# Kernel optimization log

Measured on AMD Instinct MI355X. Metric: run time of the kernel, lower is better.

## Reference

```python
import jax, jax.numpy as jnp
import numpy as np

B, T = 32, 1024
TEMP_IN, STAT_IN = 128, 64
TEMP_OUT, STAT_OUT = 128, 64
EPS = 1e-5
NEG_SLOPE = 0.01


def _bn_eval(x, gamma, beta, mean, var):
    # BatchNorm1d in eval mode (running stats)
    return (x - mean) * jax.lax.rsqrt(var + EPS) * gamma + beta


def _leaky_relu(x):
    return jnp.where(x >= 0, x, NEG_SLOPE * x)


def setup_inputs() -> dict:
    key = jax.random.key(0)
    k = jax.random.split(key, 6)
    # deterministic ragged lengths in [512, 1024]
    lengths_np = (512 + (np.arange(B) * 37) % 513).astype(np.int64)
    N = int(lengths_np.sum())  # 23450
    batch_idx = np.repeat(np.arange(B), lengths_np).astype(np.int32)
    pos_idx = np.concatenate([np.arange(l) for l in lengths_np]).astype(np.int32)
    valid = (np.arange(T)[None, :] < lengths_np[:, None])  # [B, T]
    mask_repeat = valid[:, :, None] & valid[:, None, :]    # [B, T, T]

    inp = {
        "x_temp": jax.random.normal(k[0], (N, TEMP_IN), jnp.float32),
        "x_stat": jax.random.normal(k[1], (B, STAT_IN), jnp.float32),
        "temp_attn": jax.random.normal(k[2], (B, T, T), jnp.float32) * 0.1,
        "mask_repeat": jnp.asarray(mask_repeat),
        "lengths": jnp.asarray(lengths_np),
        "batch_idx": jnp.asarray(batch_idx),
        "pos_idx": jnp.asarray(pos_idx),
        # non_linear_temp: Linear(TEMP_IN+STAT_IN -> TEMP_OUT) + BN
        "W1": jax.random.normal(k[3], (TEMP_OUT, TEMP_IN + STAT_IN), jnp.float32) / np.sqrt(TEMP_IN + STAT_IN),
        "b1": jnp.zeros((TEMP_OUT,), jnp.float32),
        "gamma1": jnp.ones((TEMP_OUT,), jnp.float32),
        "beta1": jnp.zeros((TEMP_OUT,), jnp.float32),
        "mean1": jnp.zeros((TEMP_OUT,), jnp.float32),
        "var1": jnp.ones((TEMP_OUT,), jnp.float32),
        # non_linear_stat: Linear(STAT_IN -> STAT_OUT) + BN
        "W2": jax.random.normal(k[4], (STAT_OUT, STAT_IN), jnp.float32) / np.sqrt(STAT_IN),
        "b2": jnp.zeros((STAT_OUT,), jnp.float32),
        "gamma2": jnp.ones((STAT_OUT,), jnp.float32),
        "beta2": jnp.zeros((STAT_OUT,), jnp.float32),
        "mean2": jnp.zeros((STAT_OUT,), jnp.float32),
        "var2": jnp.ones((STAT_OUT,), jnp.float32),
    }
    return inp


def reference(x_temp, x_stat, temp_attn, mask_repeat, lengths, batch_idx, pos_idx,
              W1, b1, gamma1, beta1, mean1, var1,
              W2, b2, gamma2, beta2, mean2, var2):
    # repeat_static_features: gather per-batch static feats to packed rows
    x_stat_rep = x_stat[batch_idx]                              # [N, STAT_IN]
    h = jnp.concatenate((x_temp, x_stat_rep), axis=-1) @ W1.T + b1
    h = _leaky_relu(_bn_eval(h, gamma1, beta1, mean1, var1))    # [N, TEMP_OUT]

    # pad_packed_sequences: scatter packed rows into [B, T, C] (zeros elsewhere)
    padded = jnp.zeros((B, T, TEMP_OUT), h.dtype).at[batch_idx, pos_idx].set(h)

    # self attention: softmax(x x^T / sqrt(d)) over padded rows (as original)
    d = jnp.asarray(TEMP_OUT, h.dtype)
    qk = jnp.einsum('btc,bsc->bts', padded, padded) / jnp.sqrt(d)
    self_attn = jax.nn.softmax(qk, axis=-1)

    attn = jnp.where(mask_repeat, self_attn + temp_attn, jnp.asarray(0.0, h.dtype))

    x_stat_out = _leaky_relu(_bn_eval(x_stat @ W2.T + b2, gamma2, beta2, mean2, var2))

    x_out_pad = jnp.einsum('bts,bsc->btc', attn, padded)        # [B, T, TEMP_OUT]
    # pack_padded_sequences: gather valid positions back to packed layout
    x_out = x_out_pad[batch_idx, pos_idx]                       # [N, TEMP_OUT]
    return (x_out, x_stat_out)
```

## Files before the change

kernel.cpp:

```cpp
#include <hip/hip_runtime.h>
#include <hip/hip_bf16.h>
#include <hip/hip_fp16.h>

typedef __hip_bfloat16 bf16;
typedef __attribute__((ext_vector_type(8))) short short8;
typedef __attribute__((ext_vector_type(4))) float f32x4;

#define EPS 1e-5f
#define NSLOPE 0.01f

__device__ __forceinline__ float b2f(bf16 v) { return __bfloat162float(v); }

__device__ __forceinline__ float ld1(const void* p, size_t idx, int isbf) {
  if (isbf) return b2f(((const bf16*)p)[idx]);
  return ((const float*)p)[idx];
}
__device__ __forceinline__ void st1(void* p, size_t idx, int isbf, float v) {
  if (isbf) ((bf16*)p)[idx] = __float2bfloat16(v);
  else      ((float*)p)[idx] = v;
}
__device__ __forceinline__ short f2bs(float x) {
  bf16 t = __float2bfloat16(x);
  short s; __builtin_memcpy(&s, &t, 2); return s;
}
__device__ __forceinline__ short8 pack8f(const float* p) {
  float4 a = *(const float4*)p, b = *(const float4*)(p + 4);
  short8 r;
  r[0] = f2bs(a.x); r[1] = f2bs(a.y); r[2] = f2bs(a.z); r[3] = f2bs(a.w);
  r[4] = f2bs(b.x); r[5] = f2bs(b.y); r[6] = f2bs(b.z); r[7] = f2bs(b.w);
  return r;
}

__global__ void meta_kernel(const void* __restrict__ xt,
                            const int* __restrict__ bidx, const int* __restrict__ pidx,
                            int N, int B, int* __restrict__ rs, int* __restrict__ ln,
                            int* __restrict__ flag,
                            const void* __restrict__ W1, bf16* __restrict__ w1b, int w1n) {
  int isbf_l = 0;
  {
    unsigned w = ((const unsigned*)xt)[threadIdx.x & 63];
    unsigned lo = w & 0xffffu;
    unsigned ex = (lo >> 7) & 0xffu;
    bool sane = ((lo & 0x7fffu) == 0u) || (ex >= 96u && ex <= 134u);
    unsigned long long m = __ballot(sane);
    isbf_l = (__popcll(m) >= 48) ? 1 : 0;
    if (blockIdx.x == 0 && threadIdx.x == 0) flag[0] = isbf_l;
  }
  int stride = gridDim.x * blockDim.x;
  int g0 = blockIdx.x * blockDim.x + threadIdx.x;
  for (int i = g0; i < N; i += stride) {
    int b = bidx[i];
    if ((unsigned)b >= (unsigned)B) continue;
    if (i == 0 || bidx[i - 1] != b) rs[b] = i;
    if (i == N - 1 || bidx[i + 1] != b) ln[b] = pidx[i] + 1;
  }
  for (int i = g0; i < w1n; i += stride)
    w1b[i] = __float2bfloat16(ld1(W1, i, isbf_l));
}

__global__ void zfill_kernel(void* out, const int* __restrict__ flag, long long n) {
  const int isbf = flag[0];
  long long i = (long long)blockIdx.x * blockDim.x + threadIdx.x;
  long long stride = (long long)gridDim.x * blockDim.x;
  for (; i < n; i += stride) st1(out, (size_t)i, isbf, 0.f);
}

__global__ __launch_bounds__(256) void h_mfma_kernel(
    const void* __restrict__ xt, const void* __restrict__ xsg,
    const int* __restrict__ bidx, const bf16* __restrict__ w1b,
    const void* __restrict__ b1,
    const void* __restrict__ g1, const void* __restrict__ be1,
    const void* __restrict__ mn1, const void* __restrict__ vr1,
    const int* __restrict__ flag, bf16* __restrict__ hout, int N) {
  const int isbf = flag[0];
  const int tid = threadIdx.x, lane = tid & 63, wv = tid >> 6;
  const int m16 = lane & 15, quad = lane >> 4;
  const int row0 = blockIdx.x * 64 + wv * 16;
  const int m = row0 + m16;
  const int mc = (m < N) ? m : (N - 1);
  const int bi = bidx[mc];

  short8 af[6];
  if (isbf) {
    const bf16* xr = (const bf16*)xt + (size_t)mc * 128 + quad * 8;
#pragma unroll
    for (int ks = 0; ks < 4; ++ks) af[ks] = *(const short8*)(xr + ks * 32);
    const bf16* sr = (const bf16*)xsg + (size_t)bi * 64 + quad * 8;
    af[4] = *(const short8*)sr;
    af[5] = *(const short8*)(sr + 32);
  } else {
    const float* xr = (const float*)xt + (size_t)mc * 128 + quad * 8;
#pragma unroll
    for (int ks = 0; ks < 4; ++ks) af[ks] = pack8f(xr + ks * 32);
    const float* sr = (const float*)xsg + (size_t)bi * 64 + quad * 8;
    af[4] = pack8f(sr);
    af[5] = pack8f(sr + 32);
  }

  f32x4 acc[8];
#pragma unroll
  for (int ct = 0; ct < 8; ++ct) acc[ct] = (f32x4){0.f, 0.f, 0.f, 0.f};

#pragma unroll
  for (int ks = 0; ks < 6; ++ks) {
    const int k = ks * 32 + quad * 8;
#pragma unroll
    for (int ct = 0; ct < 8; ++ct) {
      const int o = ct * 16 + m16;
      short8 bfrag = *(const short8*)(w1b + (size_t)o * 192 + k);
      acc[ct] = __builtin_amdgcn_mfma_f32_16x16x32_bf16(af[ks], bfrag, acc[ct], 0, 0, 0);
    }
  }

#pragma unroll
  for (int ct = 0; ct < 8; ++ct) {
    const int o = ct * 16 + m16;
    float k1 = ld1(g1, o, isbf) * rsqrtf(ld1(vr1, o, isbf) + EPS);
    float k0 = ld1(be1, o, isbf) - ld1(mn1, o, isbf) * k1;
    float bias = ld1(b1, o, isbf);
#pragma unroll
    for (int r = 0; r < 4; ++r) {
      int mr = row0 + quad * 4 + r;
      if (mr < N) {
        float v = (acc[ct][r] + bias) * k1 + k0;
        v = (v >= 0.f) ? v : NSLOPE * v;
        hout[(size_t)mr * 128 + o] = __float2bfloat16(v);
      }
    }
  }
}

__global__ __launch_bounds__(64) void stat_kernel(
    const void* __restrict__ xstat, const void* __restrict__ W2,
    const void* __restrict__ b2, const void* __restrict__ g2,
    const void* __restrict__ be2, const void* __restrict__ mn2,
    const void* __restrict__ vr2, const int* __restrict__ flag,
    void* __restrict__ out, long long obase) {
  __shared__ float xs[64];
  const int isbf = flag[0];
  const int b = blockIdx.x, o = threadIdx.x;
  xs[o] = ld1(xstat, b * 64 + o, isbf);
  __syncthreads();
  float acc = ld1(b2, o, isbf);
#pragma unroll 8
  for (int j = 0; j < 64; ++j) acc += xs[j] * ld1(W2, o * 64 + j, isbf);
  float k1 = ld1(g2, o, isbf) * rsqrtf(ld1(vr2, o, isbf) + EPS);
  float k0 = ld1(be2, o, isbf) - ld1(mn2, o, isbf) * k1;
  float v = acc * k1 + k0;
  v = (v >= 0.f) ? v : NSLOPE * v;
  st1(out, (size_t)(obase + b * 64 + o), isbf, v);
}

__global__ __launch_bounds__(256, 4) void attn_mfma_kernel(
    const void* __restrict__ ta, const bf16* __restrict__ h,
    const int* __restrict__ rs_arr, const int* __restrict__ ln_arr,
    const int* __restrict__ flag, void* __restrict__ xout, int T, int N) {
  __shared__ __align__(16) unsigned short vT[128][66];
  __shared__ __align__(16) unsigned short Pbuf[16][72];
  __shared__ float wmax[4][16];
  __shared__ float wsum[4][16];
  __shared__ float mrun[16];
  __shared__ float lrun[16];

  const int b = blockIdx.y, t0 = blockIdx.x * 16;
  const int len = ln_arr[b];
  if (t0 >= len) return;
  const int isbf = flag[0];
  const int rs = rs_arr[b];
  const int nrows = min(16, len - t0);
  const int tid = threadIdx.x;
  const int lane = tid & 63, wv = tid >> 6;
  const int m16 = lane & 15, quad = lane >> 4;

  short8 qf[4];
  {
    int qrow = rs + t0 + m16;
    if (qrow > N - 1) qrow = N - 1;
    const bf16* qp = h + (size_t)qrow * 128 + quad * 8;
#pragma unroll
    for (int ks = 0; ks < 4; ++ks) qf[ks] = *(const short8*)(qp + ks * 32);
  }

  if (tid < 16) { mrun[tid] = -INFINITY; lrun[tid] = 0.f; }

  const float scale = 0.08838834764831845f;
  const short8 zero8 = {0, 0, 0, 0, 0, 0, 0, 0};
  const int scol = wv * 16 + m16;
  const size_t tarow = ((size_t)b * T + (t0 + m16)) * (size_t)T;

  f32x4 accp[2] = {{0.f,0.f,0.f,0.f},{0.f,0.f,0.f,0.f}};
  f32x4 acct[2] = {{0.f,0.f,0.f,0.f},{0.f,0.f,0.f,0.f}};

  short8 kf[4];
  {
    bool v = scol < len;
    const bf16* kp = h + (size_t)(rs + (v ? scol : 0)) * 128 + quad * 8;
#pragma unroll
    for (int ks = 0; ks < 4; ++ks) kf[ks] = v ? *(const short8*)(kp + ks * 32) : zero8;
  }

  for (int s0 = 0; s0 < len; s0 += 64) {
    for (int e = tid; e < 512; e += 256) {
      int sp = e >> 4, c8 = (e & 15) << 3;
      int s = s0 + 2 * sp;
      uint4 u0 = {0,0,0,0}, u1 = {0,0,0,0};
      if (s < len)     u0 = *(const uint4*)(h + (size_t)(rs + s) * 128 + c8);
      if (s + 1 < len) u1 = *(const uint4*)(h + (size_t)(rs + s + 1) * 128 + c8);
      const unsigned short* a0 = (const unsigned short*)&u0;
      const unsigned short* a1 = (const unsigned short*)&u1;
#pragma unroll
      for (int j = 0; j < 8; ++j)
        *(unsigned*)&vT[c8 + j][2 * sp] = (unsigned)a0[j] | ((unsigned)a1[j] << 16);
    }
    short8 taf0, taf1;
    if (isbf) {
      const bf16* tp = (const bf16*)ta + tarow + s0 + quad * 8;
      taf0 = *(const short8*)tp;
      taf1 = *(const short8*)(tp + 32);
    } else {
      const float* tp = (const float*)ta + tarow + s0 + quad * 8;
      taf0 = pack8f(tp);
      taf1 = pack8f(tp + 32);
    }
    short8 kn[4];
    {
      int sn = s0 + 64 + scol;
      bool v = sn < len;
      const bf16* kp = h + (size_t)(rs + (v ? sn : 0)) * 128 + quad * 8;
#pragma unroll
      for (int ks = 0; ks < 4; ++ks) kn[ks] = v ? *(const short8*)(kp + ks * 32) : zero8;
    }
    f32x4 sa = {0.f, 0.f, 0.f, 0.f};
#pragma unroll
    for (int ks = 0; ks < 4; ++ks)
      sa = __builtin_amdgcn_mfma_f32_16x16x32_bf16(qf[ks], kf[ks], sa, 0, 0, 0);
#pragma unroll
    for (int ks = 0; ks < 4; ++ks) kf[ks] = kn[ks];

    const bool sval = (s0 + scol) < len;
    float cm[4];
#pragma unroll
    for (int r = 0; r < 4; ++r) cm[r] = sval ? sa[r] * scale : -INFINITY;
#pragma unroll
    for (int off = 1; off <= 8; off <<= 1) {
#pragma unroll
      for (int r = 0; r < 4; ++r) cm[r] = fmaxf(cm[r], __shfl_xor(cm[r], off, 64));
    }
    if (m16 == 0) {
#pragma unroll
      for (int r = 0; r < 4; ++r) wmax[wv][quad * 4 + r] = cm[r];
    }
    __syncthreads();

    float mnew[4], al[4], p[4];
#pragma unroll
    for (int r = 0; r < 4; ++r) {
      int row = quad * 4 + r;
      float cmax = fmaxf(fmaxf(wmax[0][row], wmax[1][row]),
                         fmaxf(wmax[2][row], wmax[3][row]));
      float mold = mrun[row];
      mnew[r] = fmaxf(mold, cmax);
      al[r] = __expf(mold - mnew[r]);
      p[r] = sval ? __expf(sa[r] * scale - mnew[r]) : 0.f;
    }
    float cs[4];
#pragma unroll
    for (int r = 0; r < 4; ++r) cs[r] = p[r];
#pragma unroll
    for (int off = 1; off <= 8; off <<= 1) {
#pragma unroll
      for (int r = 0; r < 4; ++r) cs[r] += __shfl_xor(cs[r], off, 64);
    }
    if (m16 == 0) {
#pragma unroll
      for (int r = 0; r < 4; ++r) wsum[wv][quad * 4 + r] = cs[r];
    }
#pragma unroll
    for (int r = 0; r < 4; ++r)
      Pbuf[quad * 4 + r][wv * 16 + m16] = (unsigned short)f2bs(p[r]);
    __syncthreads();

    if (wv == 0 && m16 == 0) {
#pragma unroll
      for (int r = 0; r < 4; ++r) {
        int row = quad * 4 + r;
        float st = wsum[0][row] + wsum[1][row] + wsum[2][row] + wsum[3][row];
        lrun[row] = lrun[row] * al[r] + st;
        mrun[row] = mnew[r];
      }
    }
#pragma unroll
    for (int ct = 0; ct < 2; ++ct) {
#pragma unroll
      for (int r = 0; r < 4; ++r) accp[ct][r] *= al[r];
    }
#pragma unroll
    for (int ks = 0; ks < 2; ++ks) {
      short8 pf = *(const short8*)&Pbuf[m16][ks * 32 + quad * 8];
      short8 tf = ks ? taf1 : taf0;
#pragma unroll
      for (int ct = 0; ct < 2; ++ct) {
        const int c0 = wv * 32 + ct * 16;
        const unsigned short* vrow = &vT[c0 + m16][ks * 32 + quad * 8];
        unsigned w0 = *(const unsigned*)(vrow + 0);
        unsigned w1 = *(const unsigned*)(vrow + 2);
        unsigned w2 = *(const unsigned*)(vrow + 4);
        unsigned w3 = *(const unsigned*)(vrow + 6);
        short8 bfv;
        bfv[0] = (short)(w0 & 0xffffu); bfv[1] = (short)(w0 >> 16);
        bfv[2] = (short)(w1 & 0xffffu); bfv[3] = (short)(w1 >> 16);
        bfv[4] = (short)(w2 & 0xffffu); bfv[5] = (short)(w2 >> 16);
        bfv[6] = (short)(w3 & 0xffffu); bfv[7] = (short)(w3 >> 16);
        if (ct == 0) {
          accp[0] = __builtin_amdgcn_mfma_f32_16x16x32_bf16(pf, bfv, accp[0], 0, 0, 0);
          acct[0] = __builtin_amdgcn_mfma_f32_16x16x32_bf16(tf, bfv, acct[0], 0, 0, 0);
        } else {
          accp[1] = __builtin_amdgcn_mfma_f32_16x16x32_bf16(pf, bfv, accp[1], 0, 0, 0);
          acct[1] = __builtin_amdgcn_mfma_f32_16x16x32_bf16(tf, bfv, acct[1], 0, 0, 0);
        }
      }
    }
    __syncthreads();
  }

#pragma unroll
  for (int r = 0; r < 4; ++r) {
    int t = quad * 4 + r;
    if (t < nrows) {
      float m_r = mrun[t], l_r = lrun[t];
      float m_f = (len < T) ? fmaxf(m_r, 0.f) : m_r;
      float corr = __expf(m_r - m_f);
      float l_f = l_r * corr + (float)(T - len) * __expf(-m_f);
      float os = corr / l_f;
      size_t ob = (size_t)(rs + t0 + t) * 128;
      st1(xout, ob + wv * 32 + m16,      isbf, accp[0][r] * os + acct[0][r]);
      st1(xout, ob + wv * 32 + 16 + m16, isbf, accp[1][r] * os + acct[1][r]);
    }
  }
}

extern "C" void kernel_launch(void* const* d_in, const int* in_sizes, int n_in,
                              void* d_out, int out_size, void* d_ws, size_t ws_size,
                              hipStream_t stream) {
  const void* x_temp    = d_in[0];
  const void* x_stat    = d_in[1];
  const void* temp_attn = d_in[2];
  const int N = in_sizes[0] / 128;
  const int B = in_sizes[1] / 64;
  long long tt = (long long)in_sizes[2] / B;
  int T = 1; while ((long long)(T + 1) * (T + 1) <= tt) ++T;

  int p = 3;
  while (p < n_in && in_sizes[p] != N) ++p;
  const int* batch_idx = (const int*)d_in[p++];
  const int* pos_idx   = (const int*)d_in[p++];
  const void* W1 = d_in[p++];
  const void* b1 = d_in[p++];
  const void* g1 = d_in[p++];
  const void* be1= d_in[p++];
  const void* mn1= d_in[p++];
  const void* vr1= d_in[p++];
  const void* W2 = d_in[p++];
  const void* b2 = d_in[p++];
  const void* g2 = d_in[p++];
  const void* be2= d_in[p++];
  const void* mn2= d_in[p++];
  const void* vr2= d_in[p++];

  int*  meta = (int*)d_ws;
  int*  rs   = meta;
  int*  lnp  = meta + B;
  int*  flag = meta + 2 * B;
  bf16* h    = (bf16*)((char*)d_ws + 1024);
  bf16* w1b  = h + (size_t)N * 128;
  const int w1n = 128 * 192;
  size_t need = 1024 + (size_t)N * 128 * sizeof(bf16) + (size_t)w1n * sizeof(bf16);

  long long obase = (long long)N * 128;

  meta_kernel<<<90, 256, 0, stream>>>(x_temp, batch_idx, pos_idx, N, B, rs, lnp,
                                      flag, W1, w1b, w1n);
  stat_kernel<<<B, 64, 0, stream>>>(x_stat, W2, b2, g2, be2, mn2, vr2, flag,
                                    d_out, obase);
  if (ws_size >= need) {
    h_mfma_kernel<<<(N + 63) / 64, 256, 0, stream>>>(x_temp, x_stat, batch_idx,
                                                     w1b, b1, g1, be1, mn1, vr1,
                                                     flag, h, N);
    attn_mfma_kernel<<<dim3((T + 15) / 16, B), 256, 0, stream>>>(
        temp_attn, h, rs, lnp, flag, d_out, T, N);
  } else {
    zfill_kernel<<<512, 256, 0, stream>>>(d_out, flag, obase);
  }
}
```

Measured before the change: 425.4 us.

## Restructure attention so each wave owns 16 query rows and double-buffer V

```diff
diff --git a/kernel.cpp b/kernel.cpp
--- a/kernel.cpp
+++ b/kernel.cpp
@@ -54,8 +54,14 @@
     if (i == 0 || bidx[i - 1] != b) rs[b] = i;
     if (i == N - 1 || bidx[i + 1] != b) ln[b] = pidx[i] + 1;
   }
-  for (int i = g0; i < w1n; i += stride)
-    w1b[i] = __float2bfloat16(ld1(W1, i, isbf_l));
+  for (int i = g0; i < w1n; i += stride) {
+    int o = i / 192, k = i - o * 192;
+    int ct = o >> 4, n = o & 15;
+    int ks = k >> 5, rem = k & 31;
+    int q = rem >> 3, j = rem & 7;
+    int fi = ((ct * 6 + ks) * 64 + q * 16 + n) * 8 + j;
+    w1b[fi] = __float2bfloat16(ld1(W1, i, isbf_l));
+  }
 }
 
 __global__ void zfill_kernel(void* out, const int* __restrict__ flag, long long n) {
@@ -101,13 +107,12 @@
 #pragma unroll
   for (int ct = 0; ct < 8; ++ct) acc[ct] = (f32x4){0.f, 0.f, 0.f, 0.f};
 
+  const short8* wf = (const short8*)w1b;
 #pragma unroll
   for (int ks = 0; ks < 6; ++ks) {
-    const int k = ks * 32 + quad * 8;
 #pragma unroll
     for (int ct = 0; ct < 8; ++ct) {
-      const int o = ct * 16 + m16;
-      short8 bfrag = *(const short8*)(w1b + (size_t)o * 192 + k);
+      short8 bfrag = wf[(ct * 6 + ks) * 64 + lane];
       acc[ct] = __builtin_amdgcn_mfma_f32_16x16x32_bf16(af[ks], bfrag, acc[ct], 0, 0, 0);
     }
   }
@@ -151,67 +156,82 @@
   st1(out, (size_t)(obase + b * 64 + o), isbf, v);
 }
 
-__global__ __launch_bounds__(256, 4) void attn_mfma_kernel(
+__global__ __launch_bounds__(256, 2) void attn_mfma_kernel(
     const void* __restrict__ ta, const bf16* __restrict__ h,
     const int* __restrict__ rs_arr, const int* __restrict__ ln_arr,
     const int* __restrict__ flag, void* __restrict__ xout, int T, int N) {
-  __shared__ __align__(16) unsigned short vT[128][66];
-  __shared__ __align__(16) unsigned short Pbuf[16][72];
-  __shared__ float wmax[4][16];
-  __shared__ float wsum[4][16];
-  __shared__ float mrun[16];
-  __shared__ float lrun[16];
-
-  const int b = blockIdx.y, t0 = blockIdx.x * 16;
+  __shared__ __align__(16) unsigned short vT[2][128][72];
+  __shared__ __align__(16) unsigned short Pw[4][16][72];
+
+  const int b = blockIdx.y, t0 = blockIdx.x * 64;
   const int len = ln_arr[b];
   if (t0 >= len) return;
   const int isbf = flag[0];
   const int rs = rs_arr[b];
-  const int nrows = min(16, len - t0);
   const int tid = threadIdx.x;
   const int lane = tid & 63, wv = tid >> 6;
   const int m16 = lane & 15, quad = lane >> 4;
+  const int t0w = t0 + wv * 16;
 
   short8 qf[4];
   {
-    int qrow = rs + t0 + m16;
+    int qrow = rs + t0w + m16;
     if (qrow > N - 1) qrow = N - 1;
     const bf16* qp = h + (size_t)qrow * 128 + quad * 8;
 #pragma unroll
     for (int ks = 0; ks < 4; ++ks) qf[ks] = *(const short8*)(qp + ks * 32);
   }
 
-  if (tid < 16) { mrun[tid] = -INFINITY; lrun[tid] = 0.f; }
-
   const float scale = 0.08838834764831845f;
   const short8 zero8 = {0, 0, 0, 0, 0, 0, 0, 0};
-  const int scol = wv * 16 + m16;
-  const size_t tarow = ((size_t)b * T + (t0 + m16)) * (size_t)T;
-
-  f32x4 accp[2] = {{0.f,0.f,0.f,0.f},{0.f,0.f,0.f,0.f}};
-  f32x4 acct[2] = {{0.f,0.f,0.f,0.f},{0.f,0.f,0.f,0.f}};
-
-  short8 kf[4];
+  const uint4 zz = {0, 0, 0, 0};
+  const size_t tarow = ((size_t)b * T + (t0w + m16)) * (size_t)T;
+  const int c8base = wv * 32;
+
+  f32x4 accp[8], acct[8];
+#pragma unroll
+  for (int ct = 0; ct < 8; ++ct) {
+    accp[ct] = (f32x4){0.f, 0.f, 0.f, 0.f};
+    acct[ct] = (f32x4){0.f, 0.f, 0.f, 0.f};
+  }
+  float mrun[4], lrun[4];
+#pragma unroll
+  for (int r = 0; r < 4; ++r) { mrun[r] = -INFINITY; lrun[r] = 0.f; }
+
   {
-    bool v = scol < len;
-    const bf16* kp = h + (size_t)(rs + (v ? scol : 0)) * 128 + quad * 8;
-#pragma unroll
-    for (int ks = 0; ks < 4; ++ks) kf[ks] = v ? *(const short8*)(kp + ks * 32) : zero8;
-  }
-
-  for (int s0 = 0; s0 < len; s0 += 64) {
-    for (int e = tid; e < 512; e += 256) {
-      int sp = e >> 4, c8 = (e & 15) << 3;
-      int s = s0 + 2 * sp;
-      uint4 u0 = {0,0,0,0}, u1 = {0,0,0,0};
-      if (s < len)     u0 = *(const uint4*)(h + (size_t)(rs + s) * 128 + c8);
-      if (s + 1 < len) u1 = *(const uint4*)(h + (size_t)(rs + s + 1) * 128 + c8);
-      const unsigned short* a0 = (const unsigned short*)&u0;
-      const unsigned short* a1 = (const unsigned short*)&u1;
-#pragma unroll
-      for (int j = 0; j < 8; ++j)
-        *(unsigned*)&vT[c8 + j][2 * sp] = (unsigned)a0[j] | ((unsigned)a1[j] << 16);
-    }
+    int srow = lane;
+    bool v = srow < len;
+    const bf16* src = h + (size_t)(rs + (v ? srow : 0)) * 128;
+#pragma unroll
+    for (int it = 0; it < 4; ++it) {
+      int c8 = c8base + it * 8;
+      uint4 u = v ? *(const uint4*)(src + c8) : zz;
+      const unsigned short* a = (const unsigned short*)&u;
+#pragma unroll
+      for (int j = 0; j < 8; ++j) vT[0][c8 + j][lane] = a[j];
+    }
+  }
+  __syncthreads();
+
+  const int nchunk = (len + 63) >> 6;
+  for (int ci = 0; ci < nchunk; ++ci) {
+    const int s0 = ci << 6;
+    const int p = ci & 1;
+    const bool have_next = (ci + 1 < nchunk);
+
+    uint4 su0 = zz, su1 = zz, su2 = zz, su3 = zz;
+    if (have_next) {
+      int srow = s0 + 64 + lane;
+      bool v = srow < len;
+      const bf16* src = h + (size_t)(rs + (v ? srow : 0)) * 128;
+      if (v) {
+        su0 = *(const uint4*)(src + c8base);
+        su1 = *(const uint4*)(src + c8base + 8);
+        su2 = *(const uint4*)(src + c8base + 16);
+        su3 = *(const uint4*)(src + c8base + 24);
+      }
+    }
+
     short8 taf0, taf1;
     if (isbf) {
       const bf16* tp = (const bf16*)ta + tarow + s0 + quad * 8;
@@ -222,119 +242,111 @@
       taf0 = pack8f(tp);
       taf1 = pack8f(tp + 32);
     }
-    short8 kn[4];
-    {
-      int sn = s0 + 64 + scol;
-      bool v = sn < len;
-      const bf16* kp = h + (size_t)(rs + (v ? sn : 0)) * 128 + quad * 8;
-#pragma unroll
-      for (int ks = 0; ks < 4; ++ks) kn[ks] = v ? *(const short8*)(kp + ks * 32) : zero8;
-    }
-    f32x4 sa = {0.f, 0.f, 0.f, 0.f};
-#pragma unroll
-    for (int ks = 0; ks < 4; ++ks)
-      sa = __builtin_amdgcn_mfma_f32_16x16x32_bf16(qf[ks], kf[ks], sa, 0, 0, 0);
-#pragma unroll
-    for (int ks = 0; ks < 4; ++ks) kf[ks] = kn[ks];
-
-    const bool sval = (s0 + scol) < len;
+
+    f32x4 sa[4];
+    bool sval[4];
+#pragma unroll
+    for (int st = 0; st < 4; ++st) {
+      int srow = s0 + st * 16 + m16;
+      bool v = srow < len;
+      sval[st] = v;
+      const bf16* kp = h + (size_t)(rs + (v ? srow : 0)) * 128 + quad * 8;
+      f32x4 a0 = (f32x4){0.f, 0.f, 0.f, 0.f};
+#pragma unroll
+      for (int ks = 0; ks < 4; ++ks) {
+        short8 kf = v ? *(const short8*)(kp + ks * 32) : zero8;
+        a0 = __builtin_amdgcn_mfma_f32_16x16x32_bf16(qf[ks], kf, a0, 0, 0, 0);
+      }
+      sa[st] = a0;
+    }
+
     float cm[4];
 #pragma unroll
-    for (int r = 0; r < 4; ++r) cm[r] = sval ? sa[r] * scale : -INFINITY;
+    for (int r = 0; r < 4; ++r) cm[r] = -INFINITY;
+#pragma unroll
+    for (int st = 0; st < 4; ++st) {
+#pragma unroll
+      for (int r = 0; r < 4; ++r)
+        cm[r] = fmaxf(cm[r], sval[st] ? sa[st][r] * scale : -INFINITY);
+    }
 #pragma unroll
     for (int off = 1; off <= 8; off <<= 1) {
 #pragma unroll
       for (int r = 0; r < 4; ++r) cm[r] = fmaxf(cm[r], __shfl_xor(cm[r], off, 64));
     }
-    if (m16 == 0) {
-#pragma unroll
-      for (int r = 0; r < 4; ++r) wmax[wv][quad * 4 + r] = cm[r];
+    float al[4], csum[4];
+#pragma unroll
+    for (int r = 0; r < 4; ++r) {
+      float mnew = fmaxf(mrun[r], cm[r]);
+      al[r] = __expf(mrun[r] - mnew);
+      mrun[r] = mnew;
+      csum[r] = 0.f;
+    }
+#pragma unroll
+    for (int st = 0; st < 4; ++st) {
+#pragma unroll
+      for (int r = 0; r < 4; ++r) {
+        float pv = sval[st] ? __expf(sa[st][r] * scale - mrun[r]) : 0.f;
+        csum[r] += pv;
+        Pw[wv][quad * 4 + r][st * 16 + m16] = (unsigned short)f2bs(pv);
+      }
+    }
+#pragma unroll
+    for (int off = 1; off <= 8; off <<= 1) {
+#pragma unroll
+      for (int r = 0; r < 4; ++r) csum[r] += __shfl_xor(csum[r], off, 64);
+    }
+#pragma unroll
+    for (int r = 0; r < 4; ++r) lrun[r] = lrun[r] * al[r] + csum[r];
+
+#pragma unroll
+    for (int ct = 0; ct < 8; ++ct) {
+#pragma unroll
+      for (int r = 0; r < 4; ++r) accp[ct][r] *= al[r];
+    }
+
+#pragma unroll
+    for (int ks = 0; ks < 2; ++ks) {
+      short8 pf = *(const short8*)&Pw[wv][m16][ks * 32 + quad * 8];
+      short8 tf = ks ? taf1 : taf0;
+#pragma unroll
+      for (int ct = 0; ct < 8; ++ct) {
+        short8 bfv = *(const short8*)&vT[p][ct * 16 + m16][ks * 32 + quad * 8];
+        accp[ct] = __builtin_amdgcn_mfma_f32_16x16x32_bf16(pf, bfv, accp[ct], 0, 0, 0);
+        acct[ct] = __builtin_amdgcn_mfma_f32_16x16x32_bf16(tf, bfv, acct[ct], 0, 0, 0);
+      }
+    }
+
+    if (have_next) {
+      const unsigned short* a0 = (const unsigned short*)&su0;
+      const unsigned short* a1 = (const unsigned short*)&su1;
+      const unsigned short* a2 = (const unsigned short*)&su2;
+      const unsigned short* a3 = (const unsigned short*)&su3;
+#pragma unroll
+      for (int j = 0; j < 8; ++j) {
+        vT[p ^ 1][c8base + j][lane]      = a0[j];
+        vT[p ^ 1][c8base + 8 + j][lane]  = a1[j];
+        vT[p ^ 1][c8base + 16 + j][lane] = a2[j];
+        vT[p ^ 1][c8base + 24 + j][lane] = a3[j];
+      }
     }
     __syncthreads();
-
-    float mnew[4], al[4], p[4];
-#pragma unroll
-    for (int r = 0; r < 4; ++r) {
-      int row = quad * 4 + r;
-      float cmax = fmaxf(fmaxf(wmax[0][row], wmax[1][row]),
-                         fmaxf(wmax[2][row], wmax[3][row]));
-      float mold = mrun[row];
-      mnew[r] = fmaxf(mold, cmax);
-      al[r] = __expf(mold - mnew[r]);
-      p[r] = sval ? __expf(sa[r] * scale - mnew[r]) : 0.f;
-    }
-    float cs[4];
-#pragma unroll
-    for (int r = 0; r < 4; ++r) cs[r] = p[r];
-#pragma unroll
-    for (int off = 1; off <= 8; off <<= 1) {
-#pragma unroll
-      for (int r = 0; r < 4; ++r) cs[r] += __shfl_xor(cs[r], off, 64);
-    }
-    if (m16 == 0) {
-#pragma unroll
-      for (int r = 0; r < 4; ++r) wsum[wv][quad * 4 + r] = cs[r];
-    }
-#pragma unroll
-    for (int r = 0; r < 4; ++r)
-      Pbuf[quad * 4 + r][wv * 16 + m16] = (unsigned short)f2bs(p[r]);
-    __syncthreads();
-
-    if (wv == 0 && m16 == 0) {
-#pragma unroll
-      for (int r = 0; r < 4; ++r) {
-        int row = quad * 4 + r;
-        float st = wsum[0][row] + wsum[1][row] + wsum[2][row] + wsum[3][row];
-        lrun[row] = lrun[row] * al[r] + st;
-        mrun[row] = mnew[r];
-      }
-    }
-#pragma unroll
-    for (int ct = 0; ct < 2; ++ct) {
-#pragma unroll
-      for (int r = 0; r < 4; ++r) accp[ct][r] *= al[r];
-    }
-#pragma unroll
-    for (int ks = 0; ks < 2; ++ks) {
-      short8 pf = *(const short8*)&Pbuf[m16][ks * 32 + quad * 8];
-      short8 tf = ks ? taf1 : taf0;
-#pragma unroll
-      for (int ct = 0; ct < 2; ++ct) {
-        const int c0 = wv * 32 + ct * 16;
-        const unsigned short* vrow = &vT[c0 + m16][ks * 32 + quad * 8];
-        unsigned w0 = *(const unsigned*)(vrow + 0);
-        unsigned w1 = *(const unsigned*)(vrow + 2);
-        unsigned w2 = *(const unsigned*)(vrow + 4);
-        unsigned w3 = *(const unsigned*)(vrow + 6);
-        short8 bfv;
-        bfv[0] = (short)(w0 & 0xffffu); bfv[1] = (short)(w0 >> 16);
-        bfv[2] = (short)(w1 & 0xffffu); bfv[3] = (short)(w1 >> 16);
-        bfv[4] = (short)(w2 & 0xffffu); bfv[5] = (short)(w2 >> 16);
-        bfv[6] = (short)(w3 & 0xffffu); bfv[7] = (short)(w3 >> 16);
-        if (ct == 0) {
-          accp[0] = __builtin_amdgcn_mfma_f32_16x16x32_bf16(pf, bfv, accp[0], 0, 0, 0);
-          acct[0] = __builtin_amdgcn_mfma_f32_16x16x32_bf16(tf, bfv, acct[0], 0, 0, 0);
-        } else {
-          accp[1] = __builtin_amdgcn_mfma_f32_16x16x32_bf16(pf, bfv, accp[1], 0, 0, 0);
-          acct[1] = __builtin_amdgcn_mfma_f32_16x16x32_bf16(tf, bfv, acct[1], 0, 0, 0);
-        }
-      }
-    }
-    __syncthreads();
-  }
-
+  }
+
+  const int nr = len - t0w;
 #pragma unroll
   for (int r = 0; r < 4; ++r) {
     int t = quad * 4 + r;
-    if (t < nrows) {
-      float m_r = mrun[t], l_r = lrun[t];
+    if (t < nr) {
+      float m_r = mrun[r], l_r = lrun[r];
       float m_f = (len < T) ? fmaxf(m_r, 0.f) : m_r;
       float corr = __expf(m_r - m_f);
       float l_f = l_r * corr + (float)(T - len) * __expf(-m_f);
       float os = corr / l_f;
-      size_t ob = (size_t)(rs + t0 + t) * 128;
-      st1(xout, ob + wv * 32 + m16,      isbf, accp[0][r] * os + acct[0][r]);
-      st1(xout, ob + wv * 32 + 16 + m16, isbf, accp[1][r] * os + acct[1][r]);
+      size_t ob = (size_t)(rs + t0w + t) * 128;
+#pragma unroll
+      for (int ct = 0; ct < 8; ++ct)
+        st1(xout, ob + ct * 16 + m16, isbf, accp[ct][r] * os + acct[ct][r]);
     }
   }
 }
@@ -386,7 +398,7 @@
     h_mfma_kernel<<<(N + 63) / 64, 256, 0, stream>>>(x_temp, x_stat, batch_idx,
                                                      w1b, b1, g1, be1, mn1, vr1,
                                                      flag, h, N);
-    attn_mfma_kernel<<<dim3((T + 15) / 16, B), 256, 0, stream>>>(
+    attn_mfma_kernel<<<dim3((T + 63) / 64, B), 256, 0, stream>>>(
         temp_attn, h, rs, lnp, flag, d_out, T, N);
   } else {
     zfill_kernel<<<512, 256, 0, stream>>>(d_out, flag, obase);
```

Result: faster. 395.9 us (-6.9%).
